# Optimization experiments

Hardware: AMD Instinct MI355X
Metric: run time of the kernel (lower is better)

Reference implementation:

```python
import jax, jax.numpy as jnp
import numpy as np

EMB = 768
BLOCK = 64
K = EMB // BLOCK  # 12


def setup_inputs() -> dict:
    key = jax.random.key(0)
    ks = jax.random.split(key, 8)
    n, c, d, h, E, M, P = 4, 1024, 768, 12, 32, 4, 256
    seq = jax.random.normal(ks[0], (n, c, d), dtype=jnp.float32)
    attn = jax.random.uniform(ks[1], (n, h, c, c), dtype=jnp.float32)
    attn = attn / attn.sum(-1, keepdims=True)  # attention-like rows
    mention_pos = jax.random.randint(ks[2], (n, E, M), 0, c)
    hts = jax.random.randint(ks[3], (n, P, 2), 0, E)
    W_head = jax.random.normal(ks[4], (2 * d, EMB), dtype=jnp.float32) / np.sqrt(2 * d)
    W_tail = jax.random.normal(ks[5], (2 * d, EMB), dtype=jnp.float32) / np.sqrt(2 * d)
    W_bil = jax.random.normal(ks[6], (EMB * BLOCK, 97), dtype=jnp.float32) / np.sqrt(EMB * BLOCK)
    return {
        "sequence_output": seq,
        "attention": attn,
        "mention_pos": mention_pos,
        "hts": hts,
        "W_head": W_head,
        "b_head": jnp.zeros((EMB,), jnp.float32),
        "W_tail": W_tail,
        "b_tail": jnp.zeros((EMB,), jnp.float32),
        "W_bil": W_bil,
        "b_bil": jnp.zeros((97,), jnp.float32),
    }


def reference(sequence_output, attention, mention_pos, hts,
              W_head, b_head, W_tail, b_tail, W_bil, b_bil):
    n, c, d = sequence_output.shape
    h = attention.shape[1]
    P = hts.shape[1]

    bidx = jnp.arange(n)[:, None, None]
    # gather mention token embeddings: [n, E, M, d]
    m_emb = sequence_output[bidx, mention_pos]
    # entity embedding = logsumexp over mentions (single-mention case is identical)
    ent_emb = jax.nn.logsumexp(m_emb, axis=2)                      # [n, E, d]

    # per-mention attention rows: attention[i, :, pos, :] -> [n, E, M, h, c]
    att_t = jnp.transpose(attention, (0, 2, 1, 3))                 # [n, c, h, c]
    m_att = att_t[bidx, mention_pos]                               # [n, E, M, h, c]
    ent_att = m_att.mean(axis=2)                                   # [n, E, h, c]

    pidx = jnp.arange(n)[:, None]
    hs = ent_emb[pidx, hts[..., 0]]                                # [n, P, d]
    ts = ent_emb[pidx, hts[..., 1]]
    h_att = ent_att[pidx, hts[..., 0]]                             # [n, P, h, c]
    t_att = ent_att[pidx, hts[..., 1]]

    ht_att = (h_att * t_att).mean(axis=2)                          # [n, P, c]
    ht_att = ht_att / (ht_att.sum(-1, keepdims=True) + 1e-30)
    # relation context: contract('ld,rl->rd') per doc
    rs = jnp.einsum('ncd,npc->npd', sequence_output, ht_att)       # [n, P, d]

    R = n * P
    hs2 = jnp.tanh(jnp.concatenate([hs, rs], -1).reshape(R, 2 * d) @ W_head + b_head)
    ts2 = jnp.tanh(jnp.concatenate([ts, rs], -1).reshape(R, 2 * d) @ W_tail + b_tail)

    b1 = hs2.reshape(R, K, BLOCK)
    b2 = ts2.reshape(R, K, BLOCK)
    bl = (b1[:, :, :, None] * b2[:, :, None, :]).reshape(R, EMB * BLOCK)
    logits = bl @ W_bil + b_bil                                    # [R, 97]
    return logits
```

## Files before the change

kernel.cpp:

```cpp
#include <hip/hip_runtime.h>
#include <hip/hip_bf16.h>
#include <math.h>

#define ND 4
#define CL 1024
#define DD 768
#define HH 12
#define EE 32
#define MMEN 4
#define PP 256
#define EMBD 768
#define KBL 12
#define OUTD 97
#define RTOT (ND*PP)
#define NSPLIT 48

typedef unsigned short u16;
typedef __attribute__((ext_vector_type(8))) short short8;
typedef __attribute__((ext_vector_type(4))) float f32x4;

static __device__ inline float bf16u_to_f(unsigned v){
  union { unsigned u; float f; } c; c.u = v << 16; return c.f;
}
static __device__ inline unsigned f_to_bf16u(float f){
  union { float f; unsigned u; } c; c.f = f;
  return (c.u + 0x7fffu + ((c.u >> 16) & 1u)) >> 16;
}

#define GLOAD_LDS16(gp, lp) __builtin_amdgcn_global_load_lds( \
    (const __attribute__((address_space(1))) unsigned*)(gp), \
    (__attribute__((address_space(3))) unsigned*)(lp), 16, 0, 0)

__global__ __launch_bounds__(256) void k_ent_emb(const float* __restrict__ seq,
    const int* __restrict__ mpos, u16* __restrict__ ent_emb_bf,
    float* __restrict__ S)
{
  int idx = blockIdx.x*256 + threadIdx.x;
  if (idx >= ND*EE*DD) return;
  if (idx < RTOT) S[idx] = 0.f;
  int dd = idx % DD;
  int e  = (idx / DD) % EE;
  int i  = idx / (DD*EE);
  const int* mp = mpos + (i*EE + e)*MMEN;
  float v[MMEN];
  float mx = -1e30f;
  #pragma unroll
  for (int m=0;m<MMEN;m++){
    v[m] = seq[(i*CL + mp[m])*DD + dd];
    mx = fmaxf(mx, v[m]);
  }
  float s = 0.f;
  #pragma unroll
  for (int m=0;m<MMEN;m++) s += expf(v[m]-mx);
  ent_emb_bf[idx] = (u16)f_to_bf16u(mx + logf(s));
}

__global__ __launch_bounds__(256) void k_ent_att(const float* __restrict__ attn,
    const int* __restrict__ mpos, u16* __restrict__ ent_att_bf)
{
  int idx = blockIdx.x*256 + threadIdx.x;
  if (idx >= ND*EE*HH*(CL/8)) return;
  int j8   = idx % (CL/8);
  int head = (idx / (CL/8)) % HH;
  int e    = (idx / (CL/8*HH)) % EE;
  int i    = idx / (CL/8*HH*EE);
  const int* mp = mpos + (i*EE + e)*MMEN;
  float acc[8] = {};
  #pragma unroll
  for (int m=0;m<MMEN;m++){
    const float4* p = (const float4*)(attn +
        ((size_t)(i*HH + head)*CL + mp[m])*CL + j8*8);
    float4 a = p[0], b = p[1];
    acc[0]+=a.x; acc[1]+=a.y; acc[2]+=a.z; acc[3]+=a.w;
    acc[4]+=b.x; acc[5]+=b.y; acc[6]+=b.z; acc[7]+=b.w;
  }
  unsigned o[4];
  #pragma unroll
  for (int q=0;q<4;q++){
    unsigned lo = f_to_bf16u(acc[2*q]   * (1.f/MMEN));
    unsigned hi = f_to_bf16u(acc[2*q+1] * (1.f/MMEN));
    o[q] = lo | (hi<<16);
  }
  ((uint4*)ent_att_bf)[idx] = make_uint4(o[0],o[1],o[2],o[3]);
}

__global__ __launch_bounds__(256) void k_ht_att(const u16* __restrict__ ent_att_bf,
    const int* __restrict__ hts, u16* __restrict__ u_ht_bf, float* __restrict__ S)
{
  const int j0  = blockIdx.x*64;
  const int pb  = blockIdx.y*64;
  const int doc = blockIdx.z;
  const int tid = threadIdx.x;
  const int p_local = tid >> 2, quad = tid & 3;
  const int grow = doc*PP + pb + p_local;
  const int he = hts[grow*2+0], te = hts[grow*2+1];
  const u16* ha = ent_att_bf + ((size_t)(doc*EE + he)*HH)*CL;
  const u16* ta = ent_att_bf + ((size_t)(doc*EE + te)*HH)*CL;
  const int jj = j0 + quad*16;

  float acc[16] = {};
  #pragma unroll
  for (int h=0; h<HH; h++){
    const uint4* pa = (const uint4*)(ha + h*CL + jj);
    const uint4* pb4 = (const uint4*)(ta + h*CL + jj);
    uint4 a0 = pa[0], a1 = pa[1];
    uint4 b0 = pb4[0], b1 = pb4[1];
    unsigned ua[8] = {a0.x,a0.y,a0.z,a0.w,a1.x,a1.y,a1.z,a1.w};
    unsigned ub[8] = {b0.x,b0.y,b0.z,b0.w,b1.x,b1.y,b1.z,b1.w};
    #pragma unroll
    for (int q=0;q<8;q++){
      acc[2*q]   += bf16u_to_f(ua[q]&0xffffu) * bf16u_to_f(ub[q]&0xffffu);
      acc[2*q+1] += bf16u_to_f(ua[q]>>16)     * bf16u_to_f(ub[q]>>16);
    }
  }
  float sum = 0.f;
  unsigned o[8];
  #pragma unroll
  for (int q=0;q<8;q++){
    float v0 = acc[2*q]   * (1.f/HH);
    float v1 = acc[2*q+1] * (1.f/HH);
    sum += v0 + v1;
    o[q] = f_to_bf16u(v0) | (f_to_bf16u(v1)<<16);
  }
  uint4* dst = (uint4*)(u_ht_bf + (size_t)grow*CL + jj);
  dst[0] = make_uint4(o[0],o[1],o[2],o[3]);
  dst[1] = make_uint4(o[4],o[5],o[6],o[7]);
  sum += __shfl_xor(sum, 1, 64);
  sum += __shfl_xor(sum, 2, 64);
  if (quad == 0) atomicAdd(&S[grow], sum);
}

__global__ __launch_bounds__(256) void k_transpose_bf(const float* __restrict__ src,
    u16* __restrict__ dst, int R, int C)
{
  size_t boff = (size_t)blockIdx.z * R * C;
  src += boff; dst += boff;
  __shared__ float t[32][33];
  int tx = threadIdx.x & 31, ty = threadIdx.x >> 5;
  int c0 = blockIdx.x*32, r0 = blockIdx.y*32;
  #pragma unroll
  for (int q=0;q<4;q++)
    t[ty+8*q][tx] = src[(size_t)(r0+ty+8*q)*C + c0+tx];
  __syncthreads();
  #pragma unroll
  for (int q=0;q<4;q++)
    dst[(size_t)(c0+ty+8*q)*R + r0+tx] = (u16)f_to_bf16u(t[tx][ty+8*q]);
}

__global__ __launch_bounds__(256) void k_transpose_bf_w(
    const float* __restrict__ srcA, u16* __restrict__ dstA,
    const float* __restrict__ srcB, u16* __restrict__ dstB, int R, int C)
{
  const float* src = blockIdx.z ? srcB : srcA;
  u16* dst         = blockIdx.z ? dstB : dstA;
  __shared__ float t[32][33];
  int tx = threadIdx.x & 31, ty = threadIdx.x >> 5;
  int c0 = blockIdx.x*32, r0 = blockIdx.y*32;
  #pragma unroll
  for (int q=0;q<4;q++)
    t[ty+8*q][tx] = src[(size_t)(r0+ty+8*q)*C + c0+tx];
  __syncthreads();
  #pragma unroll
  for (int q=0;q<4;q++)
    dst[(size_t)(c0+ty+8*q)*R + r0+tx] = (u16)f_to_bf16u(t[tx][ty+8*q]);
}

__global__ __launch_bounds__(256) void k_gemm_rs_mfma(
    const u16* __restrict__ u_ht_bf, const u16* __restrict__ seq_t_bf,
    const float* __restrict__ S, u16* __restrict__ rs_bf)
{
  const int rt = blockIdx.x, ct = blockIdx.y, doc = blockIdx.z;
  const u16* A  = u_ht_bf + (size_t)doc*PP*CL;
  const u16* Bt = seq_t_bf + (size_t)doc*DD*CL;
  const int row0 = rt*128, col0 = ct*64;
  __shared__ __align__(16) u16 As[128*32];
  __shared__ __align__(16) u16 Bs[64*32];
  const int tid = threadIdx.x, lane = tid & 63, wave = tid >> 6;
  const int m = lane & 15, j8 = lane >> 4;
  const int srow = lane >> 2, schunk = lane & 3;
  f32x4 acc[2][4];
  #pragma unroll
  for (int a=0;a<2;a++)
    #pragma unroll
    for (int b=0;b<4;b++) acc[a][b] = (f32x4){0.f,0.f,0.f,0.f};

  for (int k0 = 0; k0 < CL; k0 += 32){
    __syncthreads();
    #pragma unroll
    for (int ii=0; ii<2; ii++){
      int i = wave*2 + ii;
      int row = i*16 + srow;
      int gc = schunk ^ ((row>>1)&3);
      const u16* gp = A + (size_t)(row0+row)*CL + k0 + gc*8;
      GLOAD_LDS16(gp, &As[i*16*32]);
    }
    {
      int row = wave*16 + srow;
      int gc = schunk ^ ((row>>1)&3);
      const u16* gp = Bt + (size_t)(col0+row)*CL + k0 + gc*8;
      GLOAD_LDS16(gp, &Bs[wave*16*32]);
    }
    __syncthreads();
    short8 af[2], bf[4];
    #pragma unroll
    for (int mf=0; mf<2; mf++){
      int r = wave*32 + mf*16 + m;
      af[mf] = *(const short8*)&As[r*32 + 8*(j8 ^ ((r>>1)&3))];
    }
    #pragma unroll
    for (int nt=0; nt<4; nt++){
      int n = nt*16 + m;
      bf[nt] = *(const short8*)&Bs[n*32 + 8*(j8 ^ ((n>>1)&3))];
    }
    #pragma unroll
    for (int mf=0; mf<2; mf++)
      #pragma unroll
      for (int nt=0; nt<4; nt++)
        acc[mf][nt] = __builtin_amdgcn_mfma_f32_16x16x32_bf16(af[mf], bf[nt], acc[mf][nt], 0,0,0);
  }

  #pragma unroll
  for (int mf=0; mf<2; mf++){
    #pragma unroll
    for (int nt=0; nt<4; nt++){
      int colg = col0 + nt*16 + m;
      #pragma unroll
      for (int reg=0; reg<4; reg++){
        int rowg = doc*PP + row0 + wave*32 + mf*16 + j8*4 + reg;
        float sc = 1.f / (S[rowg] + 1e-30f);
        rs_bf[(size_t)rowg*DD + colg] = (u16)f_to_bf16u(acc[mf][nt][reg] * sc);
      }
    }
  }
}

__global__ __launch_bounds__(256) void k_gemm_ht_mfma(
    const u16* __restrict__ ent_emb_bf, const u16* __restrict__ rs_bf,
    const int* __restrict__ hts,
    const u16* __restrict__ Wht, const u16* __restrict__ Wtt,
    const float* __restrict__ b_head, const float* __restrict__ b_tail,
    u16* __restrict__ hs2b, u16* __restrict__ ts2b)
{
  const int rt = blockIdx.x, ct = blockIdx.y, z = blockIdx.z;
  const u16* Bt   = z ? Wtt : Wht;
  const float* bias = z ? b_tail : b_head;
  u16* C          = z ? ts2b : hs2b;
  const int row0 = rt*128, col0 = ct*64;
  __shared__ __align__(16) u16 As[128*32];
  __shared__ __align__(16) u16 Bs[64*32];
  const int tid = threadIdx.x, lane = tid & 63, wave = tid >> 6;
  const int m = lane & 15, j8 = lane >> 4;
  const int srow = lane >> 2, schunk = lane & 3;

  const u16* gEnt[2]; const u16* gRs[2]; int gcA[2];
  #pragma unroll
  for (int ii=0; ii<2; ii++){
    int row  = (wave*2+ii)*16 + srow;
    int grow = row0 + row;
    int ent  = hts[grow*2 + z];
    gEnt[ii] = ent_emb_bf + ((size_t)((grow>>8)*EE + ent))*DD;
    gRs[ii]  = rs_bf + (size_t)grow*DD;
    gcA[ii]  = (schunk ^ ((row>>1)&3)) * 8;
  }
  int gcB;
  {
    int row = wave*16 + srow;
    gcB = (schunk ^ ((row>>1)&3)) * 8;
  }

  f32x4 acc[2][4];
  #pragma unroll
  for (int a=0;a<2;a++)
    #pragma unroll
    for (int b=0;b<4;b++) acc[a][b] = (f32x4){0.f,0.f,0.f,0.f};

  for (int k0 = 0; k0 < 1536; k0 += 32){
    __syncthreads();
    #pragma unroll
    for (int ii=0; ii<2; ii++){
      const u16* gp = (k0 < DD) ? (gEnt[ii] + k0 + gcA[ii])
                                : (gRs[ii] + (k0-DD) + gcA[ii]);
      GLOAD_LDS16(gp, &As[(wave*2+ii)*16*32]);
    }
    {
      int row = wave*16 + srow;
      const u16* gp = Bt + (size_t)(col0+row)*1536 + k0 + gcB;
      GLOAD_LDS16(gp, &Bs[wave*16*32]);
    }
    __syncthreads();
    short8 af[2], bf[4];
    #pragma unroll
    for (int mf=0; mf<2; mf++){
      int r = wave*32 + mf*16 + m;
      af[mf] = *(const short8*)&As[r*32 + 8*(j8 ^ ((r>>1)&3))];
    }
    #pragma unroll
    for (int nt=0; nt<4; nt++){
      int n = nt*16 + m;
      bf[nt] = *(const short8*)&Bs[n*32 + 8*(j8 ^ ((n>>1)&3))];
    }
    #pragma unroll
    for (int mf=0; mf<2; mf++)
      #pragma unroll
      for (int nt=0; nt<4; nt++)
        acc[mf][nt] = __builtin_amdgcn_mfma_f32_16x16x32_bf16(af[mf], bf[nt], acc[mf][nt], 0,0,0);
  }

  #pragma unroll
  for (int mf=0; mf<2; mf++){
    #pragma unroll
    for (int nt=0; nt<4; nt++){
      int colg = col0 + nt*16 + m;
      float bv = bias[colg];
      #pragma unroll
      for (int reg=0; reg<4; reg++){
        int rowg = row0 + wave*32 + mf*16 + j8*4 + reg;
        C[(size_t)rowg*DD + colg] = (u16)f_to_bf16u(tanhf(acc[mf][nt][reg] + bv));
      }
    }
  }
}

__global__ __launch_bounds__(256) void k_wt2(const float* __restrict__ W_bil,
    u16* __restrict__ Wt2)
{
  const int cc = blockIdx.x;
  __shared__ u16 lds2[4480];
  int tid = threadIdx.x;
  for (int u=tid; u<4480; u+=256) lds2[u] = 0;
  __syncthreads();
  for (int u=tid; u<112*32; u+=256){
    int kk = u / 112, n = u % 112;
    if (n < OUTD)
      lds2[n*40 + kk] = (u16)f_to_bf16u(W_bil[(size_t)(cc*32 + kk)*OUTD + n]);
  }
  __syncthreads();
  uint4* dst = (uint4*)(Wt2 + (size_t)cc*4480);
  const uint4* src = (const uint4*)lds2;
  for (int v=tid; v<560; v+=256) dst[v] = src[v];
}

__global__ __launch_bounds__(256) void k_bilinear(
    const u16* __restrict__ hs2b, const u16* __restrict__ ts2b,
    const u16* __restrict__ Wt2, float* __restrict__ pbuf)
{
  const int rt = blockIdx.x;
  const int sp = blockIdx.y;
  const int kb = sp >> 2;
  const int i0 = (sp & 3) * 16;
  const int row0 = rt * 128;

  __shared__ __align__(16) u16 b1s[128][24];
  __shared__ __align__(16) u16 b2s[128][72];
  __shared__ __align__(16) u16 Ws[4480];

  const int tid = threadIdx.x;
  const int lane = tid & 63, wave = tid >> 6;
  const int m = lane & 15, j8 = lane >> 4;

  {
    int r = tid >> 1, half = tid & 1;
    uint4 v = *(const uint4*)&hs2b[(size_t)(row0+r)*EMBD + kb*64 + i0 + half*8];
    *(uint4*)&b1s[r][half*8] = v;
  }
  for (int u=tid; u<1024; u+=256){
    int r = u >> 3, seg = u & 7;
    uint4 v = *(const uint4*)&ts2b[(size_t)(row0+r)*EMBD + kb*64 + seg*8];
    *(uint4*)&b2s[r][seg*8] = v;
  }

  const uint4* gsrc = (const uint4*)(Wt2 + (size_t)(sp*32)*4480);
  uint4* ws4 = (uint4*)Ws;
  uint4 pf0, pf1, pf2;
  {
    pf0 = gsrc[tid];
    pf1 = gsrc[tid+256];
    if (tid < 48) pf2 = gsrc[tid+512];
  }

  f32x4 acc[2][7];
  #pragma unroll
  for (int f=0;f<2;f++)
    #pragma unroll
    for (int nt=0;nt<7;nt++) acc[f][nt] = (f32x4){0.f,0.f,0.f,0.f};

  for (int c=0; c<32; c++){
    __syncthreads();
    ws4[tid] = pf0; ws4[tid+256] = pf1; if (tid < 48) ws4[tid+512] = pf2;
    if (c+1 < 32){
      size_t b = (size_t)(c+1)*560;
      pf0 = gsrc[b+tid];
      pf1 = gsrc[b+tid+256];
      if (tid < 48) pf2 = gsrc[b+tid+512];
    }
    __syncthreads();

    const int i_rel = c >> 1;
    const int j0 = (c & 1) * 32;

    short8 bfr[7];
    #pragma unroll
    for (int nt=0;nt<7;nt++)
      bfr[nt] = *(const short8*)&Ws[(nt*16 + m)*40 + j8*8];

    #pragma unroll
    for (int f=0;f<2;f++){
      int r = wave*32 + f*16 + m;
      float s = bf16u_to_f(b1s[r][i_rel]);
      uint4 u = *(const uint4*)&b2s[r][j0 + j8*8];
      unsigned uw[4] = {u.x, u.y, u.z, u.w};
      short8 af;
      #pragma unroll
      for (int e=0;e<4;e++){
        af[2*e]   = (short)f_to_bf16u(s * bf16u_to_f(uw[e] & 0xffffu));
        af[2*e+1] = (short)f_to_bf16u(s * bf16u_to_f(uw[e] >> 16));
      }
      #pragma unroll
      for (int nt=0;nt<7;nt++)
        acc[f][nt] = __builtin_amdgcn_mfma_f32_16x16x32_bf16(af, bfr[nt], acc[f][nt], 0, 0, 0);
    }
  }

  float* dst = pbuf + ((size_t)sp*RTOT + row0)*112;
  #pragma unroll
  for (int f=0;f<2;f++){
    #pragma unroll
    for (int nt=0;nt<7;nt++){
      int col = nt*16 + m;
      #pragma unroll
      for (int reg=0;reg<4;reg++){
        int lrow = wave*32 + f*16 + j8*4 + reg;
        dst[(size_t)lrow*112 + col] = acc[f][nt][reg];
      }
    }
  }
}

__global__ __launch_bounds__(256) void k_reduce_logits(
    const float* __restrict__ pbuf, const float* __restrict__ b_bil,
    float* __restrict__ logits)
{
  int idx = blockIdx.x*256 + threadIdx.x;
  if (idx >= RTOT*112) return;
  int col = idx % 112, row = idx / 112;
  if (col >= OUTD) return;
  float s0 = 0.f, s1 = 0.f, s2 = 0.f, s3 = 0.f;
  const size_t stride = (size_t)RTOT*112;
  #pragma unroll
  for (int sp=0; sp<NSPLIT; sp+=4){
    s0 += pbuf[(sp+0)*stride + idx];
    s1 += pbuf[(sp+1)*stride + idx];
    s2 += pbuf[(sp+2)*stride + idx];
    s3 += pbuf[(sp+3)*stride + idx];
  }
  logits[(size_t)row*OUTD + col] = (s0+s1) + (s2+s3) + b_bil[col];
}

extern "C" void kernel_launch(void* const* d_in, const int* in_sizes, int n_in,
                              void* d_out, int out_size, void* d_ws, size_t ws_size,
                              hipStream_t stream)
{
  const float* seq    = (const float*)d_in[0];
  const float* attn   = (const float*)d_in[1];
  const int*   mpos   = (const int*)d_in[2];
  const int*   hts    = (const int*)d_in[3];
  const float* W_head = (const float*)d_in[4];
  const float* b_head = (const float*)d_in[5];
  const float* W_tail = (const float*)d_in[6];
  const float* b_tail = (const float*)d_in[7];
  const float* W_bil  = (const float*)d_in[8];
  const float* b_bil  = (const float*)d_in[9];
  float* logits = (float*)d_out;

  float* ws = (float*)d_ws;
  u16*   ent_emb_bf = (u16*)(ws + 0);
  float* S          = ws + 49152;
  u16*   rs_bf      = (u16*)(ws + 50176);
  u16*   hs2b       = (u16*)(ws + 443392);
  u16*   ts2b       = (u16*)(ws + 836608);
  u16*   Wh_t       = (u16*)(ws + 1229824);
  u16*   Wt_t       = (u16*)(ws + 1819648);
  u16*   ent_att_bf = (u16*)(ws + 2409472);
  u16*   u_ht_bf    = (u16*)(ws + 3195904);
  u16*   seq_t_bf   = (u16*)(ws + 3720192);
  u16*   Wt2        = (u16*)(ws + 5293056);
  float* pbuf       = ws + 8733696;

  k_ent_emb<<<(ND*EE*DD+255)/256, 256, 0, stream>>>(seq, mpos, ent_emb_bf, S);
  k_ent_att<<<(ND*EE*HH*(CL/8)+255)/256, 256, 0, stream>>>(attn, mpos, ent_att_bf);
  k_ht_att<<<dim3(16, 4, 4), 256, 0, stream>>>(ent_att_bf, hts, u_ht_bf, S);
  k_transpose_bf<<<dim3(DD/32, CL/32, ND), 256, 0, stream>>>(seq, seq_t_bf, CL, DD);
  k_transpose_bf_w<<<dim3(DD/32, 1536/32, 2), 256, 0, stream>>>(
      W_head, Wh_t, W_tail, Wt_t, 1536, DD);
  k_gemm_rs_mfma<<<dim3(2, 12, 4), 256, 0, stream>>>(u_ht_bf, seq_t_bf, S, rs_bf);
  k_gemm_ht_mfma<<<dim3(8, 12, 2), 256, 0, stream>>>(ent_emb_bf, rs_bf, hts,
      Wh_t, Wt_t, b_head, b_tail, hs2b, ts2b);
  k_wt2<<<1536, 256, 0, stream>>>(W_bil, Wt2);
  k_bilinear<<<dim3(RTOT/128, NSPLIT), 256, 0, stream>>>(hs2b, ts2b, Wt2, pbuf);
  k_reduce_logits<<<(RTOT*112+255)/256, 256, 0, stream>>>(pbuf, b_bil, logits);
}
```

Before: 367.9 us.

## Use fp16 for bilinear operands and widen GEMM K-tiles to 64

Switches the hs2/ts2 activations and the transposed W_bil to fp16, so the bilinear kernel builds its outer-product A fragments with a packed half8 multiply instead of per-element bf16 unpack/convert, and uses the f16 MFMA. Separately, the rs and head/tail GEMMs now stage 64-wide K tiles with an 8-chunk XOR swizzle, halving the number of barrier pairs per K loop. The fp16 change trades bf16's range for more mantissa; tanh outputs and small weights fit fp16, but the product s*b2 is now rounded in fp16. The larger tiles double LDS use per block.

Measured after the change: 359.3 us. 1.02x faster.

```diff
diff --git a/kernel.cpp b/kernel.cpp
--- a/kernel.cpp
+++ b/kernel.cpp
@@ -17,6 +17,7 @@
 
 typedef unsigned short u16;
 typedef __attribute__((ext_vector_type(8))) short short8;
+typedef __attribute__((ext_vector_type(8))) _Float16 half8;
 typedef __attribute__((ext_vector_type(4))) float f32x4;
 
 static __device__ inline float bf16u_to_f(unsigned v){
@@ -25,6 +26,10 @@
 static __device__ inline unsigned f_to_bf16u(float f){
   union { float f; unsigned u; } c; c.f = f;
   return (c.u + 0x7fffu + ((c.u >> 16) & 1u)) >> 16;
+}
+static __device__ inline u16 f_to_f16u(float f){
+  _Float16 h = (_Float16)f;
+  union { _Float16 h; u16 u; } c; c.h = h; return c.u;
 }
 
 #define GLOAD_LDS16(gp, lp) __builtin_amdgcn_global_load_lds( \
@@ -173,50 +178,55 @@
   const u16* A  = u_ht_bf + (size_t)doc*PP*CL;
   const u16* Bt = seq_t_bf + (size_t)doc*DD*CL;
   const int row0 = rt*128, col0 = ct*64;
-  __shared__ __align__(16) u16 As[128*32];
-  __shared__ __align__(16) u16 Bs[64*32];
+  __shared__ __align__(16) u16 As[128*64];
+  __shared__ __align__(16) u16 Bs[64*64];
   const int tid = threadIdx.x, lane = tid & 63, wave = tid >> 6;
   const int m = lane & 15, j8 = lane >> 4;
-  const int srow = lane >> 2, schunk = lane & 3;
+  const int srow8 = lane >> 3, sc8 = lane & 7;
   f32x4 acc[2][4];
   #pragma unroll
   for (int a=0;a<2;a++)
     #pragma unroll
     for (int b=0;b<4;b++) acc[a][b] = (f32x4){0.f,0.f,0.f,0.f};
 
-  for (int k0 = 0; k0 < CL; k0 += 32){
+  for (int k0 = 0; k0 < CL; k0 += 64){
     __syncthreads();
     #pragma unroll
+    for (int ii=0; ii<4; ii++){
+      int row = ii*32 + wave*8 + srow8;
+      int gc = sc8 ^ (row & 7);
+      const u16* gp = A + (size_t)(row0+row)*CL + k0 + gc*8;
+      GLOAD_LDS16(gp, &As[(ii*32 + wave*8)*64]);
+    }
+    #pragma unroll
     for (int ii=0; ii<2; ii++){
-      int i = wave*2 + ii;
-      int row = i*16 + srow;
-      int gc = schunk ^ ((row>>1)&3);
-      const u16* gp = A + (size_t)(row0+row)*CL + k0 + gc*8;
-      GLOAD_LDS16(gp, &As[i*16*32]);
-    }
-    {
-      int row = wave*16 + srow;
-      int gc = schunk ^ ((row>>1)&3);
+      int row = ii*32 + wave*8 + srow8;
+      int gc = sc8 ^ (row & 7);
       const u16* gp = Bt + (size_t)(col0+row)*CL + k0 + gc*8;
-      GLOAD_LDS16(gp, &Bs[wave*16*32]);
+      GLOAD_LDS16(gp, &Bs[(ii*32 + wave*8)*64]);
     }
     __syncthreads();
-    short8 af[2], bf[4];
-    #pragma unroll
-    for (int mf=0; mf<2; mf++){
-      int r = wave*32 + mf*16 + m;
-      af[mf] = *(const short8*)&As[r*32 + 8*(j8 ^ ((r>>1)&3))];
-    }
-    #pragma unroll
-    for (int nt=0; nt<4; nt++){
-      int n = nt*16 + m;
-      bf[nt] = *(const short8*)&Bs[n*32 + 8*(j8 ^ ((n>>1)&3))];
-    }
-    #pragma unroll
-    for (int mf=0; mf<2; mf++)
-      #pragma unroll
-      for (int nt=0; nt<4; nt++)
-        acc[mf][nt] = __builtin_amdgcn_mfma_f32_16x16x32_bf16(af[mf], bf[nt], acc[mf][nt], 0,0,0);
+    #pragma unroll
+    for (int h=0; h<2; h++){
+      short8 af[2], bf[4];
+      #pragma unroll
+      for (int mf=0; mf<2; mf++){
+        int r = wave*32 + mf*16 + m;
+        int c = (h*4 + j8) ^ (r & 7);
+        af[mf] = *(const short8*)&As[r*64 + c*8];
+      }
+      #pragma unroll
+      for (int nt=0; nt<4; nt++){
+        int n = nt*16 + m;
+        int c = (h*4 + j8) ^ (n & 7);
+        bf[nt] = *(const short8*)&Bs[n*64 + c*8];
+      }
+      #pragma unroll
+      for (int mf=0; mf<2; mf++)
+        #pragma unroll
+        for (int nt=0; nt<4; nt++)
+          acc[mf][nt] = __builtin_amdgcn_mfma_f32_16x16x32_bf16(af[mf], bf[nt], acc[mf][nt], 0,0,0);
+    }
   }
 
   #pragma unroll
@@ -239,33 +249,28 @@
     const int* __restrict__ hts,
     const u16* __restrict__ Wht, const u16* __restrict__ Wtt,
     const float* __restrict__ b_head, const float* __restrict__ b_tail,
-    u16* __restrict__ hs2b, u16* __restrict__ ts2b)
+    u16* __restrict__ hs2h, u16* __restrict__ ts2h)
 {
   const int rt = blockIdx.x, ct = blockIdx.y, z = blockIdx.z;
   const u16* Bt   = z ? Wtt : Wht;
   const float* bias = z ? b_tail : b_head;
-  u16* C          = z ? ts2b : hs2b;
+  u16* C          = z ? ts2h : hs2h;
   const int row0 = rt*128, col0 = ct*64;
-  __shared__ __align__(16) u16 As[128*32];
-  __shared__ __align__(16) u16 Bs[64*32];
+  __shared__ __align__(16) u16 As[128*64];
+  __shared__ __align__(16) u16 Bs[64*64];
   const int tid = threadIdx.x, lane = tid & 63, wave = tid >> 6;
   const int m = lane & 15, j8 = lane >> 4;
-  const int srow = lane >> 2, schunk = lane & 3;
-
-  const u16* gEnt[2]; const u16* gRs[2]; int gcA[2];
-  #pragma unroll
-  for (int ii=0; ii<2; ii++){
-    int row  = (wave*2+ii)*16 + srow;
+  const int srow8 = lane >> 3, sc8 = lane & 7;
+
+  const u16* gEnt[4]; const u16* gRs[4]; int gcA[4];
+  #pragma unroll
+  for (int ii=0; ii<4; ii++){
+    int row  = ii*32 + wave*8 + srow8;
     int grow = row0 + row;
     int ent  = hts[grow*2 + z];
     gEnt[ii] = ent_emb_bf + ((size_t)((grow>>8)*EE + ent))*DD;
     gRs[ii]  = rs_bf + (size_t)grow*DD;
-    gcA[ii]  = (schunk ^ ((row>>1)&3)) * 8;
-  }
-  int gcB;
-  {
-    int row = wave*16 + srow;
-    gcB = (schunk ^ ((row>>1)&3)) * 8;
+    gcA[ii]  = (sc8 ^ (row & 7)) * 8;
   }
 
   f32x4 acc[2][4];
@@ -274,36 +279,43 @@
     #pragma unroll
     for (int b=0;b<4;b++) acc[a][b] = (f32x4){0.f,0.f,0.f,0.f};
 
-  for (int k0 = 0; k0 < 1536; k0 += 32){
+  for (int k0 = 0; k0 < 1536; k0 += 64){
     __syncthreads();
     #pragma unroll
-    for (int ii=0; ii<2; ii++){
+    for (int ii=0; ii<4; ii++){
       const u16* gp = (k0 < DD) ? (gEnt[ii] + k0 + gcA[ii])
                                 : (gRs[ii] + (k0-DD) + gcA[ii]);
-      GLOAD_LDS16(gp, &As[(wave*2+ii)*16*32]);
-    }
-    {
-      int row = wave*16 + srow;
-      const u16* gp = Bt + (size_t)(col0+row)*1536 + k0 + gcB;
-      GLOAD_LDS16(gp, &Bs[wave*16*32]);
+      GLOAD_LDS16(gp, &As[(ii*32 + wave*8)*64]);
+    }
+    #pragma unroll
+    for (int ii=0; ii<2; ii++){
+      int row = ii*32 + wave*8 + srow8;
+      int gc = sc8 ^ (row & 7);
+      const u16* gp = Bt + (size_t)(col0+row)*1536 + k0 + gc*8;
+      GLOAD_LDS16(gp, &Bs[(ii*32 + wave*8)*64]);
     }
     __syncthreads();
-    short8 af[2], bf[4];
-    #pragma unroll
-    for (int mf=0; mf<2; mf++){
-      int r = wave*32 + mf*16 + m;
-      af[mf] = *(const short8*)&As[r*32 + 8*(j8 ^ ((r>>1)&3))];
-    }
-    #pragma unroll
-    for (int nt=0; nt<4; nt++){
-      int n = nt*16 + m;
-      bf[nt] = *(const short8*)&Bs[n*32 + 8*(j8 ^ ((n>>1)&3))];
-    }
-    #pragma unroll
-    for (int mf=0; mf<2; mf++)
-      #pragma unroll
-      for (int nt=0; nt<4; nt++)
-        acc[mf][nt] = __builtin_amdgcn_mfma_f32_16x16x32_bf16(af[mf], bf[nt], acc[mf][nt], 0,0,0);
+    #pragma unroll
+    for (int h=0; h<2; h++){
+      short8 af[2], bf[4];
+      #pragma unroll
+      for (int mf=0; mf<2; mf++){
+        int r = wave*32 + mf*16 + m;
+        int c = (h*4 + j8) ^ (r & 7);
+        af[mf] = *(const short8*)&As[r*64 + c*8];
+      }
+      #pragma unroll
+      for (int nt=0; nt<4; nt++){
+        int n = nt*16 + m;
+        int c = (h*4 + j8) ^ (n & 7);
+        bf[nt] = *(const short8*)&Bs[n*64 + c*8];
+      }
+      #pragma unroll
+      for (int mf=0; mf<2; mf++)
+        #pragma unroll
+        for (int nt=0; nt<4; nt++)
+          acc[mf][nt] = __builtin_amdgcn_mfma_f32_16x16x32_bf16(af[mf], bf[nt], acc[mf][nt], 0,0,0);
+    }
   }
 
   #pragma unroll
@@ -315,7 +327,7 @@
       #pragma unroll
       for (int reg=0; reg<4; reg++){
         int rowg = row0 + wave*32 + mf*16 + j8*4 + reg;
-        C[(size_t)rowg*DD + colg] = (u16)f_to_bf16u(tanhf(acc[mf][nt][reg] + bv));
+        C[(size_t)rowg*DD + colg] = f_to_f16u(tanhf(acc[mf][nt][reg] + bv));
       }
     }
   }
@@ -332,7 +344,7 @@
   for (int u=tid; u<112*32; u+=256){
     int kk = u / 112, n = u % 112;
     if (n < OUTD)
-      lds2[n*40 + kk] = (u16)f_to_bf16u(W_bil[(size_t)(cc*32 + kk)*OUTD + n]);
+      lds2[n*40 + kk] = f_to_f16u(W_bil[(size_t)(cc*32 + kk)*OUTD + n]);
   }
   __syncthreads();
   uint4* dst = (uint4*)(Wt2 + (size_t)cc*4480);
@@ -341,7 +353,7 @@
 }
 
 __global__ __launch_bounds__(256) void k_bilinear(
-    const u16* __restrict__ hs2b, const u16* __restrict__ ts2b,
+    const u16* __restrict__ hs2h, const u16* __restrict__ ts2h,
     const u16* __restrict__ Wt2, float* __restrict__ pbuf)
 {
   const int rt = blockIdx.x;
@@ -360,12 +372,12 @@
 
   {
     int r = tid >> 1, half = tid & 1;
-    uint4 v = *(const uint4*)&hs2b[(size_t)(row0+r)*EMBD + kb*64 + i0 + half*8];
+    uint4 v = *(const uint4*)&hs2h[(size_t)(row0+r)*EMBD + kb*64 + i0 + half*8];
     *(uint4*)&b1s[r][half*8] = v;
   }
   for (int u=tid; u<1024; u+=256){
     int r = u >> 3, seg = u & 7;
-    uint4 v = *(const uint4*)&ts2b[(size_t)(row0+r)*EMBD + kb*64 + seg*8];
+    uint4 v = *(const uint4*)&ts2h[(size_t)(row0+r)*EMBD + kb*64 + seg*8];
     *(uint4*)&b2s[r][seg*8] = v;
   }
 
@@ -398,26 +410,21 @@
     const int i_rel = c >> 1;
     const int j0 = (c & 1) * 32;
 
-    short8 bfr[7];
+    half8 bfr[7];
     #pragma unroll
     for (int nt=0;nt<7;nt++)
-      bfr[nt] = *(const short8*)&Ws[(nt*16 + m)*40 + j8*8];
+      bfr[nt] = *(const half8*)&Ws[(nt*16 + m)*40 + j8*8];
 
     #pragma unroll
     for (int f=0;f<2;f++){
       int r = wave*32 + f*16 + m;
-      float s = bf16u_to_f(b1s[r][i_rel]);
-      uint4 u = *(const uint4*)&b2s[r][j0 + j8*8];
-      unsigned uw[4] = {u.x, u.y, u.z, u.w};
-      short8 af;
-      #pragma unroll
-      for (int e=0;e<4;e++){
-        af[2*e]   = (short)f_to_bf16u(s * bf16u_to_f(uw[e] & 0xffffu));
-        af[2*e+1] = (short)f_to_bf16u(s * bf16u_to_f(uw[e] >> 16));
-      }
+      _Float16 s = *(const _Float16*)&b1s[r][i_rel];
+      half8 sv = {s,s,s,s,s,s,s,s};
+      half8 b2v = *(const half8*)&b2s[r][j0 + j8*8];
+      half8 af = sv * b2v;
       #pragma unroll
       for (int nt=0;nt<7;nt++)
-        acc[f][nt] = __builtin_amdgcn_mfma_f32_16x16x32_bf16(af, bfr[nt], acc[f][nt], 0, 0, 0);
+        acc[f][nt] = __builtin_amdgcn_mfma_f32_16x16x32_f16(af, bfr[nt], acc[f][nt], 0, 0, 0);
     }
   }
 
@@ -476,8 +483,8 @@
   u16*   ent_emb_bf = (u16*)(ws + 0);
   float* S          = ws + 49152;
   u16*   rs_bf      = (u16*)(ws + 50176);
-  u16*   hs2b       = (u16*)(ws + 443392);
-  u16*   ts2b       = (u16*)(ws + 836608);
+  u16*   hs2h       = (u16*)(ws + 443392);
+  u16*   ts2h       = (u16*)(ws + 836608);
   u16*   Wh_t       = (u16*)(ws + 1229824);
   u16*   Wt_t       = (u16*)(ws + 1819648);
   u16*   ent_att_bf = (u16*)(ws + 2409472);
@@ -494,8 +501,8 @@
       W_head, Wh_t, W_tail, Wt_t, 1536, DD);
   k_gemm_rs_mfma<<<dim3(2, 12, 4), 256, 0, stream>>>(u_ht_bf, seq_t_bf, S, rs_bf);
   k_gemm_ht_mfma<<<dim3(8, 12, 2), 256, 0, stream>>>(ent_emb_bf, rs_bf, hts,
-      Wh_t, Wt_t, b_head, b_tail, hs2b, ts2b);
+      Wh_t, Wt_t, b_head, b_tail, hs2h, ts2h);
   k_wt2<<<1536, 256, 0, stream>>>(W_bil, Wt2);
-  k_bilinear<<<dim3(RTOT/128, NSPLIT), 256, 0, stream>>>(hs2b, ts2b, Wt2, pbuf);
+  k_bilinear<<<dim3(RTOT/128, NSPLIT), 256, 0, stream>>>(hs2h, ts2h, Wt2, pbuf);
   k_reduce_logits<<<(RTOT*112+255)/256, 256, 0, stream>>>(pbuf, b_bil, logits);
 }
```
